# Kernel optimization log

Hardware: AMD Instinct MI355X
Metric: run time of the kernel (lower is better)

The kernel has to match this reference:

```python
import jax, jax.numpy as jnp
import numpy as np
from math import factorial

L_MAX = 3

def _cg(l1, l2, l3, m1, m2, m3):
    # Racah formula for Clebsch-Gordan coefficient <l1 m1 l2 m2 | l3 m3>
    if m1 + m2 != m3:
        return 0.0
    if l3 < abs(l1 - l2) or l3 > l1 + l2:
        return 0.0
    if abs(m1) > l1 or abs(m2) > l2 or abs(m3) > l3:
        return 0.0
    f = factorial
    pref = ((2 * l3 + 1) * f(l3 + l1 - l2) * f(l3 - l1 + l2) * f(l1 + l2 - l3) / f(l1 + l2 + l3 + 1)) ** 0.5
    pref *= (f(l3 + m3) * f(l3 - m3) * f(l1 - m1) * f(l1 + m1) * f(l2 - m2) * f(l2 + m2)) ** 0.5
    s = 0.0
    for k in range(0, l1 + l2 - l3 + 1):
        args = [k, l1 + l2 - l3 - k, l1 - m1 - k, l2 + m2 - k, l3 - l2 + m1 + k, l3 - l1 - m2 + k]
        if min(args) < 0:
            continue
        d = 1
        for a in args:
            d *= f(a)
        s += (-1) ** k / d
    return pref * s

def _build_cg_mats(l_max):
    # dense CG matrices C[(l1,l2,l3)] of shape (2l1+1, 2l2+1, 2l3+1)
    mats = {}
    for l1 in range(l_max + 1):
        for l2 in range(l_max + 1):
            for l3 in range(abs(l1 - l2), min(l1 + l2, l_max) + 1):
                C = np.zeros((2 * l1 + 1, 2 * l2 + 1, 2 * l3 + 1), dtype=np.float32)
                for m1 in range(-l1, l1 + 1):
                    for m2 in range(-l2, l2 + 1):
                        m3 = m1 + m2
                        if abs(m3) <= l3:
                            c = _cg(l1, l2, l3, m1, m2, m3)
                            if abs(c) > 1e-10:  # matches original thresholding
                                C[m1 + l1, m2 + l2, m3 + l3] = c
                mats[(l1, l2, l3)] = jnp.asarray(C)
    return mats

CG_MATS = _build_cg_mats(L_MAX)

def setup_inputs() -> dict:
    key = jax.random.key(0)
    N, C = 20000, 128
    inp = {}
    ks = jax.random.split(key, 8)
    i = 0
    for tag in ("f1", "f2"):
        for l in range(L_MAX + 1):
            inp[f"{tag}_l{l}"] = jax.random.normal(ks[i], (N, C, 2 * l + 1), dtype=jnp.float32)
            i += 1
    return inp

def reference(f1_l0, f1_l1, f1_l2, f1_l3, f2_l0, f2_l1, f2_l2, f2_l3):
    f1 = {0: f1_l0, 1: f1_l1, 2: f1_l2, 3: f1_l3}
    f2 = {0: f2_l0, 1: f2_l1, 2: f2_l2, 3: f2_l3}
    out = {l3: None for l3 in range(L_MAX + 1)}
    for l1 in range(L_MAX + 1):
        for l2 in range(L_MAX + 1):
            for l3 in range(abs(l1 - l2), min(l1 + l2, L_MAX) + 1):
                C = CG_MATS[(l1, l2, l3)]
                # [N,Ch,2l1+1] x [N,Ch,2l2+1] x [2l1+1,2l2+1,2l3+1] -> [N,Ch,2l3+1]
                t = jnp.einsum('nci,ncj,ijk->nck', f1[l1], f2[l2], C)
                out[l3] = t if out[l3] is None else out[l3] + t
    # concatenate l3=0..3 outputs along last dim: [N, Ch, 1+3+5+7=16]
    return jnp.concatenate([out[l3] for l3 in range(L_MAX + 1)], axis=-1)
```

## Files before the change

kernel.cpp:

```cpp
#include <hip/hip_runtime.h>
#include <hip/hip_bf16.h>


constexpr int L_MAX = 3;

constexpr double cfact(int n) {
    double r = 1.0;
    for (int i = 2; i <= n; ++i) r *= (double)i;
    return r;
}

constexpr double csqrt(double x) {
    if (x <= 0.0) return 0.0;
    double r = x > 1.0 ? x : 1.0;
    for (int i = 0; i < 80; ++i) r = 0.5 * (r + x / r);
    return r;
}

constexpr int iabs(int x) { return x < 0 ? -x : x; }

constexpr double cg(int l1, int l2, int l3, int m1, int m2) {
    int m3 = m1 + m2;
    if (l3 < iabs(l1 - l2) || l3 > l1 + l2) return 0.0;
    if (iabs(m1) > l1 || iabs(m2) > l2 || iabs(m3) > l3) return 0.0;
    double pref = csqrt((double)(2 * l3 + 1) * cfact(l3 + l1 - l2) * cfact(l3 - l1 + l2) *
                        cfact(l1 + l2 - l3) / cfact(l1 + l2 + l3 + 1));
    pref *= csqrt(cfact(l3 + m3) * cfact(l3 - m3) * cfact(l1 - m1) * cfact(l1 + m1) *
                  cfact(l2 - m2) * cfact(l2 + m2));
    double s = 0.0;
    for (int k = 0; k <= l1 + l2 - l3; ++k) {
        int a1 = k;
        int a2 = l1 + l2 - l3 - k;
        int a3 = l1 - m1 - k;
        int a4 = l2 + m2 - k;
        int a5 = l3 - l2 + m1 + k;
        int a6 = l3 - l1 - m2 + k;
        if (a1 < 0 || a2 < 0 || a3 < 0 || a4 < 0 || a5 < 0 || a6 < 0) continue;
        double d = cfact(a1) * cfact(a2) * cfact(a3) * cfact(a4) * cfact(a5) * cfact(a6);
        s += ((k & 1) ? -1.0 : 1.0) / d;
    }
    return pref * s;
}

struct Ent { int i, j, k; float c; };

constexpr int MAXE = 800;

struct Table {
    Ent e[MAXE];
    int n;
};

constexpr Table build_table() {
    Table t{};
    t.n = 0;
    int off[4] = {0, 1, 4, 9};
    for (int l1 = 0; l1 <= L_MAX; ++l1)
        for (int l2 = 0; l2 <= L_MAX; ++l2) {
            int lo = iabs(l1 - l2);
            int hi = (l1 + l2 < L_MAX) ? (l1 + l2) : L_MAX;
            for (int l3 = lo; l3 <= hi; ++l3)
                for (int m1 = -l1; m1 <= l1; ++m1)
                    for (int m2 = -l2; m2 <= l2; ++m2) {
                        int m3 = m1 + m2;
                        if (iabs(m3) > l3) continue;
                        double c = cg(l1, l2, l3, m1, m2);
                        if (c > 1e-10 || c < -1e-10) {
                            t.e[t.n].i = off[l1] + (m1 + l1);
                            t.e[t.n].j = off[l2] + (m2 + l2);
                            t.e[t.n].k = off[l3] + (m3 + l3);
                            t.e[t.n].c = (float)c;
                            t.n++;
                        }
                    }
        }
    return t;
}

constexpr Table TBL = build_table();
constexpr int TBL_N = TBL.n;

constexpr int    P_TOT  = 20000 * 128;
constexpr int    BLOCK  = 256;
constexpr int    GRID   = 2048;
constexpr size_t STRIDE = (size_t)GRID * BLOCK;

__global__ __launch_bounds__(BLOCK) void tp_kernel(
    const float* __restrict__ f1_0, const float* __restrict__ f1_1,
    const float* __restrict__ f1_2, const float* __restrict__ f1_3,
    const float* __restrict__ f2_0, const float* __restrict__ f2_1,
    const float* __restrict__ f2_2, const float* __restrict__ f2_3,
    float* __restrict__ out)
{
    for (size_t p = (size_t)blockIdx.x * BLOCK + threadIdx.x; p < (size_t)P_TOT;
         p += STRIDE) {

        float F1[16], F2[16];

        F1[0] = f1_0[p];
        F2[0] = f2_0[p];
        {
            const float* a = f1_1 + p * 3;
            const float* b = f2_1 + p * 3;
#pragma unroll
            for (int m = 0; m < 3; ++m) { F1[1 + m] = a[m]; F2[1 + m] = b[m]; }
        }
        {
            const float* a = f1_2 + p * 5;
            const float* b = f2_2 + p * 5;
#pragma unroll
            for (int m = 0; m < 5; ++m) { F1[4 + m] = a[m]; F2[4 + m] = b[m]; }
        }
        {
            const float* a = f1_3 + p * 7;
            const float* b = f2_3 + p * 7;
#pragma unroll
            for (int m = 0; m < 7; ++m) { F1[9 + m] = a[m]; F2[9 + m] = b[m]; }
        }

        float o[16];
#pragma unroll
        for (int k = 0; k < 16; ++k) o[k] = 0.0f;

#pragma unroll
        for (int e = 0; e < TBL_N; ++e) {
            o[TBL.e[e].k] = fmaf(F1[TBL.e[e].i] * F2[TBL.e[e].j], TBL.e[e].c, o[TBL.e[e].k]);
        }

        float4* op = reinterpret_cast<float4*>(out + p * 16);
        op[0] = make_float4(o[0],  o[1],  o[2],  o[3]);
        op[1] = make_float4(o[4],  o[5],  o[6],  o[7]);
        op[2] = make_float4(o[8],  o[9],  o[10], o[11]);
        op[3] = make_float4(o[12], o[13], o[14], o[15]);
    }
}

extern "C" void kernel_launch(void* const* d_in, const int* in_sizes, int n_in,
                              void* d_out, int out_size, void* d_ws, size_t ws_size,
                              hipStream_t stream) {
    const float* f1_0 = (const float*)d_in[0];
    const float* f1_1 = (const float*)d_in[1];
    const float* f1_2 = (const float*)d_in[2];
    const float* f1_3 = (const float*)d_in[3];
    const float* f2_0 = (const float*)d_in[4];
    const float* f2_1 = (const float*)d_in[5];
    const float* f2_2 = (const float*)d_in[6];
    const float* f2_3 = (const float*)d_in[7];
    float* out = (float*)d_out;

    tp_kernel<<<GRID, BLOCK, 0, stream>>>(f1_0, f1_1, f1_2, f1_3,
                                          f2_0, f2_1, f2_2, f2_3, out);
}
```

Measured before the change: 114.6 us.

## Software-pipeline feature loads with double-buffered fragments and exact grid tiling

Replaces the grid-stride loop with a fixed-trip loop (1000 blocks x 10 iterations covering exactly all 2.56M points) that prefetches the next point's 32 input floats into a second register fragment while the current one is computed and stored. The goal is to hide global-load latency behind the FMA chain and drop bounds checks. It adds launch_bounds min-blocks 4, which caps registers, and doubles the live fragment registers. This risks spills and hardcodes the problem size.

```diff
diff --git a/kernel.cpp b/kernel.cpp
--- a/kernel.cpp
+++ b/kernel.cpp
@@ -82,56 +82,78 @@
 
 constexpr int    P_TOT  = 20000 * 128;
 constexpr int    BLOCK  = 256;
-constexpr int    GRID   = 2048;
+constexpr int    GRID   = 1000;
 constexpr size_t STRIDE = (size_t)GRID * BLOCK;
+constexpr int    ITERS  = 10;
 
-__global__ __launch_bounds__(BLOCK) void tp_kernel(
+struct Frag { float f1[16]; float f2[16]; };
+
+__device__ __forceinline__ void load_frag(
+    Frag& F, size_t p,
+    const float* __restrict__ f1_0, const float* __restrict__ f1_1,
+    const float* __restrict__ f1_2, const float* __restrict__ f1_3,
+    const float* __restrict__ f2_0, const float* __restrict__ f2_1,
+    const float* __restrict__ f2_2, const float* __restrict__ f2_3)
+{
+    F.f1[0] = f1_0[p];
+    F.f2[0] = f2_0[p];
+    const float* a1 = f1_1 + p * 3;
+    const float* b1 = f2_1 + p * 3;
+#pragma unroll
+    for (int m = 0; m < 3; ++m) { F.f1[1 + m] = a1[m]; F.f2[1 + m] = b1[m]; }
+    const float* a2 = f1_2 + p * 5;
+    const float* b2 = f2_2 + p * 5;
+#pragma unroll
+    for (int m = 0; m < 5; ++m) { F.f1[4 + m] = a2[m]; F.f2[4 + m] = b2[m]; }
+    const float* a3 = f1_3 + p * 7;
+    const float* b3 = f2_3 + p * 7;
+#pragma unroll
+    for (int m = 0; m < 7; ++m) { F.f1[9 + m] = a3[m]; F.f2[9 + m] = b3[m]; }
+}
+
+__device__ __forceinline__ void compute_store(const Frag& F, size_t p,
+                                              float* __restrict__ out)
+{
+    float o[16];
+#pragma unroll
+    for (int k = 0; k < 16; ++k) o[k] = 0.0f;
+
+#pragma unroll
+    for (int e = 0; e < TBL_N; ++e) {
+        o[TBL.e[e].k] = fmaf(F.f1[TBL.e[e].i] * F.f2[TBL.e[e].j], TBL.e[e].c,
+                             o[TBL.e[e].k]);
+    }
+
+    float4* op = reinterpret_cast<float4*>(out + p * 16);
+    op[0] = make_float4(o[0],  o[1],  o[2],  o[3]);
+    op[1] = make_float4(o[4],  o[5],  o[6],  o[7]);
+    op[2] = make_float4(o[8],  o[9],  o[10], o[11]);
+    op[3] = make_float4(o[12], o[13], o[14], o[15]);
+}
+
+__global__ __launch_bounds__(BLOCK, 4) void tp_kernel(
     const float* __restrict__ f1_0, const float* __restrict__ f1_1,
     const float* __restrict__ f1_2, const float* __restrict__ f1_3,
     const float* __restrict__ f2_0, const float* __restrict__ f2_1,
     const float* __restrict__ f2_2, const float* __restrict__ f2_3,
     float* __restrict__ out)
 {
-    for (size_t p = (size_t)blockIdx.x * BLOCK + threadIdx.x; p < (size_t)P_TOT;
-         p += STRIDE) {
+    size_t p = (size_t)blockIdx.x * BLOCK + threadIdx.x;
 
-        float F1[16], F2[16];
+    Frag A, B;
 
-        F1[0] = f1_0[p];
-        F2[0] = f2_0[p];
-        {
-            const float* a = f1_1 + p * 3;
-            const float* b = f2_1 + p * 3;
-#pragma unroll
-            for (int m = 0; m < 3; ++m) { F1[1 + m] = a[m]; F2[1 + m] = b[m]; }
+    load_frag(A, p, f1_0, f1_1, f1_2, f1_3, f2_0, f2_1, f2_2, f2_3);
+
+    for (int it = 0; it < ITERS; it += 2) {
+        load_frag(B, p + STRIDE, f1_0, f1_1, f1_2, f1_3, f2_0, f2_1, f2_2, f2_3);
+        compute_store(A, p, out);
+
+        if (it + 2 < ITERS) {
+            load_frag(A, p + 2 * STRIDE, f1_0, f1_1, f1_2, f1_3, f2_0, f2_1, f2_2, f2_3);
         }
-        {
-            const float* a = f1_2 + p * 5;
-            const float* b = f2_2 + p * 5;
-#pragma unroll
-            for (int m = 0; m < 5; ++m) { F1[4 + m] = a[m]; F2[4 + m] = b[m]; }
-        }
-        {
-            const float* a = f1_3 + p * 7;
-            const float* b = f2_3 + p * 7;
-#pragma unroll
-            for (int m = 0; m < 7; ++m) { F1[9 + m] = a[m]; F2[9 + m] = b[m]; }
-        }
+        compute_store(B, p + STRIDE, out);
 
-        float o[16];
-#pragma unroll
-        for (int k = 0; k < 16; ++k) o[k] = 0.0f;
-
-#pragma unroll
-        for (int e = 0; e < TBL_N; ++e) {
-            o[TBL.e[e].k] = fmaf(F1[TBL.e[e].i] * F2[TBL.e[e].j], TBL.e[e].c, o[TBL.e[e].k]);
-        }
-
-        float4* op = reinterpret_cast<float4*>(out + p * 16);
-        op[0] = make_float4(o[0],  o[1],  o[2],  o[3]);
-        op[1] = make_float4(o[4],  o[5],  o[6],  o[7]);
-        op[2] = make_float4(o[8],  o[9],  o[10], o[11]);
-        op[3] = make_float4(o[12], o[13], o[14], o[15]);
+        p += 2 * STRIDE;
     }
 }
 
```

After: 249.9 us. 118% more time.
